# Kernel optimization log

Hardware: AMD Instinct MI355X
Metric: run time of the kernel (lower is better)

The kernel has to match this reference:

```python
import jax, jax.numpy as jnp
import numpy as np

B, K, VDIM, QDIM, NHID, SE_INNER = 8192, 6, 2048, 1024, 1024, 128

def setup_inputs() -> dict:
    key = jax.random.key(0)
    ks = jax.random.split(key, 10)
    w = lambda k, shape: jax.random.normal(k, shape, dtype=jnp.float32) * 0.02
    return {
        "v": jax.random.normal(ks[0], (B, K, VDIM), dtype=jnp.float32),
        "q": jax.random.normal(ks[1], (B, QDIM), dtype=jnp.float32),
        "mask": (jax.random.uniform(ks[2], (B, K)) > 0.5).astype(jnp.float32),
        "W1": w(ks[3], (NHID, VDIM + QDIM)),   # FCNet weight-normed Linear (effective weight)
        "b1": jnp.zeros((NHID,), jnp.float32),
        "Wl": w(ks[4], (1, NHID)),             # logits Linear(num_hid, 1)
        "bl": jnp.zeros((1,), jnp.float32),
        "Wse1": w(ks[5], (SE_INNER, 1)),       # SELayer fc1, no bias
        "Wse2": w(ks[6], (1, SE_INNER)),       # SELayer fc2, no bias
        "Wf": w(ks[7], (VDIM, 1)),             # final_att_proj Linear(1, v_dim)
        "bf": jnp.zeros((VDIM,), jnp.float32),
    }

def reference(v, q, mask, W1, b1, Wl, bl, Wse1, Wse2, Wf, bf):
    Bn, Kn, _ = v.shape
    # logits(v, q): concat q to every object, FCNet (Linear+ReLU), Linear->1 (dropout is identity at eval)
    qe = jnp.broadcast_to(q[:, None, :], (Bn, Kn, q.shape[-1]))
    vq = jnp.concatenate([v, qe], axis=-1)                       # [B,K,vd+qd]
    joint = jax.nn.relu(jnp.einsum('bkf,hf->bkh', vq, W1) + b1)  # [B,K,NHID]
    logits = jnp.einsum('bkh,oh->bko', joint, Wl) + bl           # [B,K,1]
    single_att = jax.nn.softmax(logits, axis=1)
    w = logits                                                   # view(mask_b, 6, -1) is identity here
    w_ctx = w * mask[..., None]                                  # [B,K,1]
    # per-role sum over the 5 complementary roles == total - self (exact complement index sets)
    neigh = jnp.sum(w_ctx, axis=1, keepdims=True) - w_ctx        # [B,K,1]
    x = neigh[..., None]                                         # [B,K,1,1]
    # SE gate: FC(1->128) -> ReLU -> FC(128->1) -> Sigmoid; out = x * (1 - y)
    y = jax.nn.sigmoid(jax.nn.relu(x @ Wse1.T) @ Wse2.T)          # [B,K,1,1]
    gated = x * (1.0 - y)
    # final_att_proj(gated + w[:,role].unsqueeze(-1)) : Linear(1 -> v_dim)
    upd = (gated + w[..., None]) @ Wf.T + bf                     # [B,K,1,VDIM]
    context_erased_att = upd.reshape(Bn * Kn, 1, upd.shape[-1])  # [B*K,1,VDIM]
    return single_att, context_erased_att
```

## Files before the change

kernel.cpp:

```cpp
#include <hip/hip_runtime.h>

#define B_SZ   8192
#define KOBJ   6
#define VD     2048
#define QD     1024
#define NHID_  1024
#define SEIN   128
#define M_TOT  (B_SZ * KOBJ)
#define K_TOT  (VD + QD)

typedef __bf16 bf16x8 __attribute__((ext_vector_type(8)));
typedef float  f32x4  __attribute__((ext_vector_type(4)));
typedef unsigned int uint4v __attribute__((ext_vector_type(4)));

__device__ __forceinline__ unsigned short f2bf(float f) {
    unsigned u = __builtin_bit_cast(unsigned, f);
    u += 0x7fffu + ((u >> 16) & 1u);
    return (unsigned short)(u >> 16);
}

__global__ __launch_bounds__(256) void conv_bf16(const float* __restrict__ src,
                                                 unsigned short* __restrict__ dst,
                                                 int n8) {
    int i = blockIdx.x * 256 + threadIdx.x;
    if (i < n8) {
        float4 f0 = ((const float4*)src)[2 * i];
        float4 f1 = ((const float4*)src)[2 * i + 1];
        uint4v d;
        d[0] = (unsigned)f2bf(f0.x) | ((unsigned)f2bf(f0.y) << 16);
        d[1] = (unsigned)f2bf(f0.z) | ((unsigned)f2bf(f0.w) << 16);
        d[2] = (unsigned)f2bf(f1.x) | ((unsigned)f2bf(f1.y) << 16);
        d[3] = (unsigned)f2bf(f1.z) | ((unsigned)f2bf(f1.w) << 16);
        ((uint4v*)dst)[i] = d;
    }
}

__global__ __launch_bounds__(256) void gemm_q(
    const unsigned short* __restrict__ qb, const unsigned short* __restrict__ W1b,
    const float* __restrict__ b1, float* __restrict__ Gq)
{
    __shared__ unsigned short At[128 * 32];
    __shared__ unsigned short Bt[128 * 32];

    const int tid  = threadIdx.x;
    const int bid  = blockIdx.x;
    const int nb   = bid & 7;
    const int mb   = bid >> 3;
    const int m0   = mb * 128;
    const int n0   = nb * 128;
    const int wave = tid >> 6, lane = tid & 63;
    const int quad = lane >> 4, l16 = lane & 15;
    const int wr   = (wave >> 1) * 64, wc = (wave & 1) * 64;

    const unsigned short* ga[2];
    const unsigned short* gb[2];
    unsigned short* ldsA[2];
    unsigned short* ldsB[2];
    #pragma unroll
    for (int c = 0; c < 2; ++c) {
        int seg = wave * 2 + c;
        int row = seg * 16 + (lane >> 2);
        int ch  = (lane & 3) ^ ((row >> 1) & 3);
        ga[c]   = qb + (size_t)(m0 + row) * QD + ch * 8;
        gb[c]   = W1b + (size_t)(n0 + row) * K_TOT + VD + ch * 8;
        ldsA[c] = &At[seg * 512];
        ldsB[c] = &Bt[seg * 512];
    }

    f32x4 acc[4][4] = {};
    const int swz = (l16 >> 1) & 3;

    for (int kk = 0; kk < QD; kk += 32) {
        __syncthreads();
        #pragma unroll
        for (int c = 0; c < 2; ++c)
            __builtin_amdgcn_global_load_lds(
                (const __attribute__((address_space(1))) void*)(ga[c] + kk),
                (__attribute__((address_space(3))) void*)ldsA[c], 16, 0, 0);
        #pragma unroll
        for (int c = 0; c < 2; ++c)
            __builtin_amdgcn_global_load_lds(
                (const __attribute__((address_space(1))) void*)(gb[c] + kk),
                (__attribute__((address_space(3))) void*)ldsB[c], 16, 0, 0);
        __syncthreads();

        bf16x8 af[4], bfr[4];
        #pragma unroll
        for (int i = 0; i < 4; ++i)
            af[i] = __builtin_bit_cast(bf16x8,
                *(const uint4v*)&At[(wr + i * 16 + l16) * 32 + ((quad ^ swz) * 8)]);
        #pragma unroll
        for (int j = 0; j < 4; ++j)
            bfr[j] = __builtin_bit_cast(bf16x8,
                *(const uint4v*)&Bt[(wc + j * 16 + l16) * 32 + ((quad ^ swz) * 8)]);
        #pragma unroll
        for (int i = 0; i < 4; ++i)
            #pragma unroll
            for (int j = 0; j < 4; ++j)
                acc[i][j] = __builtin_amdgcn_mfma_f32_16x16x32_bf16(af[i], bfr[j], acc[i][j], 0, 0, 0);
    }

    #pragma unroll
    for (int i = 0; i < 4; ++i)
        #pragma unroll
        for (int j = 0; j < 4; ++j) {
            int n = n0 + wc + j * 16 + l16;
            float bv = b1[n];
            #pragma unroll
            for (int r = 0; r < 4; ++r) {
                int m = m0 + wr + i * 16 + quad * 4 + r;
                Gq[(size_t)m * NHID_ + n] = acc[i][j][r] + bv;
            }
        }
}

__global__ __launch_bounds__(256) void gemm_logits(
    const unsigned short* __restrict__ vb, const unsigned short* __restrict__ W1b,
    const float* __restrict__ Gq, const float* __restrict__ Wl,
    float* __restrict__ logits)
{
    __shared__ unsigned short At[128 * 32];
    __shared__ unsigned short Bt[128 * 32];

    const int tid  = threadIdx.x;
    const int bid  = blockIdx.x;
    const int nb   = bid & 7;
    const int mb   = bid >> 3;
    const int m0   = mb * 128;
    const int n0   = nb * 128;
    const int wave = tid >> 6, lane = tid & 63;
    const int quad = lane >> 4, l16 = lane & 15;
    const int wr   = (wave >> 1) * 64, wc = (wave & 1) * 64;

    const unsigned short* gav[2];
    const unsigned short* gb[2];
    unsigned short* ldsA[2];
    unsigned short* ldsB[2];
    #pragma unroll
    for (int c = 0; c < 2; ++c) {
        int seg = wave * 2 + c;
        int row = seg * 16 + (lane >> 2);
        int ch  = (lane & 3) ^ ((row >> 1) & 3);
        gav[c]  = vb + (size_t)(m0 + row) * VD + ch * 8;
        gb[c]   = W1b + (size_t)(n0 + row) * K_TOT + ch * 8;
        ldsA[c] = &At[seg * 512];
        ldsB[c] = &Bt[seg * 512];
    }

    f32x4 acc[4][4] = {};
    const int swz = (l16 >> 1) & 3;

    for (int kk = 0; kk < VD; kk += 32) {
        __syncthreads();
        #pragma unroll
        for (int c = 0; c < 2; ++c)
            __builtin_amdgcn_global_load_lds(
                (const __attribute__((address_space(1))) void*)(gav[c] + kk),
                (__attribute__((address_space(3))) void*)ldsA[c], 16, 0, 0);
        #pragma unroll
        for (int c = 0; c < 2; ++c)
            __builtin_amdgcn_global_load_lds(
                (const __attribute__((address_space(1))) void*)(gb[c] + kk),
                (__attribute__((address_space(3))) void*)ldsB[c], 16, 0, 0);
        __syncthreads();

        bf16x8 af[4], bfr[4];
        #pragma unroll
        for (int i = 0; i < 4; ++i)
            af[i] = __builtin_bit_cast(bf16x8,
                *(const uint4v*)&At[(wr + i * 16 + l16) * 32 + ((quad ^ swz) * 8)]);
        #pragma unroll
        for (int j = 0; j < 4; ++j)
            bfr[j] = __builtin_bit_cast(bf16x8,
                *(const uint4v*)&Bt[(wc + j * 16 + l16) * 32 + ((quad ^ swz) * 8)]);
        #pragma unroll
        for (int i = 0; i < 4; ++i)
            #pragma unroll
            for (int j = 0; j < 4; ++j)
                acc[i][j] = __builtin_amdgcn_mfma_f32_16x16x32_bf16(af[i], bfr[j], acc[i][j], 0, 0, 0);
    }

    #pragma unroll
    for (int i = 0; i < 4; ++i) {
        #pragma unroll
        for (int r = 0; r < 4; ++r) {
            int m = m0 + wr + i * 16 + quad * 4 + r;
            const float* gqr = Gq + (size_t)(m / KOBJ) * NHID_;
            float sum = 0.f;
            #pragma unroll
            for (int j = 0; j < 4; ++j) {
                int n = n0 + wc + j * 16 + l16;
                float h = fmaxf(acc[i][j][r] + gqr[n], 0.f);
                sum = fmaf(h, Wl[n], sum);
            }
            sum += __shfl_xor(sum, 1);
            sum += __shfl_xor(sum, 2);
            sum += __shfl_xor(sum, 4);
            sum += __shfl_xor(sum, 8);
            if (l16 == 0) atomicAdd(&logits[m], sum);
        }
    }
}

__global__ __launch_bounds__(256) void se_kernel(
    const float* __restrict__ logits, const float* __restrict__ mask,
    const float* __restrict__ bl,
    const float* __restrict__ Wse1, const float* __restrict__ Wse2,
    float* __restrict__ out_att, float* __restrict__ s_buf)
{
    int b = blockIdx.x * 256 + threadIdx.x;
    if (b >= B_SZ) return;
    float w[KOBJ];
    float blv = bl[0];
    #pragma unroll
    for (int k = 0; k < KOBJ; ++k) w[k] = logits[b * KOBJ + k] + blv;

    float mx = w[0];
    #pragma unroll
    for (int k = 1; k < KOBJ; ++k) mx = fmaxf(mx, w[k]);
    float e[KOBJ], den = 0.f;
    #pragma unroll
    for (int k = 0; k < KOBJ; ++k) { e[k] = __expf(w[k] - mx); den += e[k]; }
    float rden = 1.f / den;
    #pragma unroll
    for (int k = 0; k < KOBJ; ++k) out_att[b * KOBJ + k] = e[k] * rden;

    float wcm[KOBJ], tot = 0.f;
    #pragma unroll
    for (int k = 0; k < KOBJ; ++k) { wcm[k] = w[k] * mask[b * KOBJ + k]; tot += wcm[k]; }

    #pragma unroll
    for (int k = 0; k < KOBJ; ++k) {
        float x = tot - wcm[k];
        float a = 0.f;
        for (int i = 0; i < SEIN; ++i)
            a = fmaf(fmaxf(x * Wse1[i], 0.f), Wse2[i], a);
        float y = 1.f / (1.f + __expf(-a));
        s_buf[b * KOBJ + k] = x * (1.f - y) + w[k];
    }
}

__global__ __launch_bounds__(256) void out_writer(
    const float* __restrict__ s_buf, const float* __restrict__ Wf,
    const float* __restrict__ bfv, float* __restrict__ out)
{
    int m = blockIdx.x;
    float s = s_buf[m];
    const float4* wf4 = (const float4*)Wf;
    const float4* bf4 = (const float4*)bfv;
    float4* o4 = (float4*)(out + (size_t)m * VD);
    #pragma unroll
    for (int it = 0; it < VD / 4 / 256; ++it) {
        int t = threadIdx.x + it * 256;
        float4 wv = wf4[t], bv = bf4[t];
        float4 r;
        r.x = fmaf(s, wv.x, bv.x);
        r.y = fmaf(s, wv.y, bv.y);
        r.z = fmaf(s, wv.z, bv.z);
        r.w = fmaf(s, wv.w, bv.w);
        o4[t] = r;
    }
}

extern "C" void kernel_launch(void* const* d_in, const int* in_sizes, int n_in,
                              void* d_out, int out_size, void* d_ws, size_t ws_size,
                              hipStream_t stream) {
    const float* v    = (const float*)d_in[0];
    const float* q    = (const float*)d_in[1];
    const float* mask = (const float*)d_in[2];
    const float* W1   = (const float*)d_in[3];
    const float* b1   = (const float*)d_in[4];
    const float* Wl   = (const float*)d_in[5];
    const float* bl   = (const float*)d_in[6];
    const float* Wse1 = (const float*)d_in[7];
    const float* Wse2 = (const float*)d_in[8];
    const float* Wf   = (const float*)d_in[9];
    const float* bfv  = (const float*)d_in[10];
    float* out = (float*)d_out;

    char* ws = (char*)d_ws;
    unsigned short* W1b = (unsigned short*)ws;
    float* logits = (float*)(ws + 6291456);
    float* s_buf  = (float*)(ws + 6291456 + 196608);

    unsigned short* vb = (unsigned short*)((char*)d_out + (size_t)M_TOT * 4);
    unsigned short* qb = (unsigned short*)((char*)d_out + (size_t)M_TOT * 4 + 201326592);
    float* Gq = (float*)((char*)d_out + (size_t)M_TOT * 4 + 201326592 + 16777216);

    hipMemsetAsync(logits, 0, M_TOT * sizeof(float), stream);
    conv_bf16<<<(NHID_ * K_TOT / 8 + 255) / 256, 256, 0, stream>>>(W1, W1b, NHID_ * K_TOT / 8);
    conv_bf16<<<(B_SZ * QD / 8 + 255) / 256, 256, 0, stream>>>(q, qb, B_SZ * QD / 8);
    gemm_q<<<(B_SZ / 128) * (NHID_ / 128), 256, 0, stream>>>(qb, W1b, b1, Gq);
    conv_bf16<<<(M_TOT * VD / 8 + 255) / 256, 256, 0, stream>>>(v, vb, M_TOT * VD / 8);
    gemm_logits<<<(M_TOT / 128) * (NHID_ / 128), 256, 0, stream>>>(vb, W1b, Gq, Wl, logits);
    se_kernel<<<(B_SZ + 255) / 256, 256, 0, stream>>>(logits, mask, bl, Wse1, Wse2, out, s_buf);
    out_writer<<<M_TOT, 256, 0, stream>>>(s_buf, Wf, bfv, out + M_TOT);
}
```

Before: 1.062 ms.

## Fuse fp32-to-bf16 conversion of v into logits GEMM and remap blocks per XCD

Drops the separate pass that converts v to bf16. The logits GEMM now reads fp32 v directly, converts it in registers and writes bf16 into LDS, which removes a 400MB read and 200MB write round trip. Block indices are also remapped so each XCD handles a contiguous range of M tiles and all 8 N tiles, improving L2 reuse of v rows. The trade-off is that A-tile loads become synchronous register loads instead of async global-to-LDS, and each block reads the fp32 v tile for all 8 N blocks, which doubles the bytes per tile compared with the bf16 copy.

Measured after the change: 1.038 ms. -2.2%, faster.

```diff
diff --git a/kernel.cpp b/kernel.cpp
--- a/kernel.cpp
+++ b/kernel.cpp
@@ -11,6 +11,7 @@
 
 typedef __bf16 bf16x8 __attribute__((ext_vector_type(8)));
 typedef float  f32x4  __attribute__((ext_vector_type(4)));
+typedef float  f32x8  __attribute__((ext_vector_type(8)));
 typedef unsigned int uint4v __attribute__((ext_vector_type(4)));
 
 __device__ __forceinline__ unsigned short f2bf(float f) {
@@ -115,7 +116,7 @@
 }
 
 __global__ __launch_bounds__(256) void gemm_logits(
-    const unsigned short* __restrict__ vb, const unsigned short* __restrict__ W1b,
+    const float* __restrict__ v, const unsigned short* __restrict__ W1b,
     const float* __restrict__ Gq, const float* __restrict__ Wl,
     float* __restrict__ logits)
 {
@@ -124,26 +125,28 @@
 
     const int tid  = threadIdx.x;
     const int bid  = blockIdx.x;
-    const int nb   = bid & 7;
-    const int mb   = bid >> 3;
-    const int m0   = mb * 128;
-    const int n0   = nb * 128;
+    const int xcd = bid & 7;
+    const int j   = bid >> 3;
+    const int nb  = j & 7;
+    const int mb  = xcd * 48 + (j >> 3);
+    const int m0  = mb * 128;
+    const int n0  = nb * 128;
     const int wave = tid >> 6, lane = tid & 63;
     const int quad = lane >> 4, l16 = lane & 15;
     const int wr   = (wave >> 1) * 64, wc = (wave & 1) * 64;
 
-    const unsigned short* gav[2];
+    const float* gav[2];
+    unsigned short* ldsAw[2];
     const unsigned short* gb[2];
-    unsigned short* ldsA[2];
     unsigned short* ldsB[2];
     #pragma unroll
     for (int c = 0; c < 2; ++c) {
         int seg = wave * 2 + c;
         int row = seg * 16 + (lane >> 2);
         int ch  = (lane & 3) ^ ((row >> 1) & 3);
-        gav[c]  = vb + (size_t)(m0 + row) * VD + ch * 8;
+        gav[c]  = v + (size_t)(m0 + row) * VD + ch * 8;
+        ldsAw[c] = &At[seg * 512 + lane * 8];
         gb[c]   = W1b + (size_t)(n0 + row) * K_TOT + ch * 8;
-        ldsA[c] = &At[seg * 512];
         ldsB[c] = &Bt[seg * 512];
     }
 
@@ -152,16 +155,26 @@
 
     for (int kk = 0; kk < VD; kk += 32) {
         __syncthreads();
-        #pragma unroll
-        for (int c = 0; c < 2; ++c)
-            __builtin_amdgcn_global_load_lds(
-                (const __attribute__((address_space(1))) void*)(gav[c] + kk),
-                (__attribute__((address_space(3))) void*)ldsA[c], 16, 0, 0);
         #pragma unroll
         for (int c = 0; c < 2; ++c)
             __builtin_amdgcn_global_load_lds(
                 (const __attribute__((address_space(1))) void*)(gb[c] + kk),
                 (__attribute__((address_space(3))) void*)ldsB[c], 16, 0, 0);
+        float4 a0[2], a1[2];
+        #pragma unroll
+        for (int c = 0; c < 2; ++c) {
+            const float4* p = (const float4*)(gav[c] + kk);
+            a0[c] = p[0];
+            a1[c] = p[1];
+        }
+        #pragma unroll
+        for (int c = 0; c < 2; ++c) {
+            f32x8 f;
+            f[0] = a0[c].x; f[1] = a0[c].y; f[2] = a0[c].z; f[3] = a0[c].w;
+            f[4] = a1[c].x; f[5] = a1[c].y; f[6] = a1[c].z; f[7] = a1[c].w;
+            bf16x8 w = __builtin_convertvector(f, bf16x8);
+            *(uint4v*)ldsAw[c] = __builtin_bit_cast(uint4v, w);
+        }
         __syncthreads();
 
         bf16x8 af[4], bfr[4];
@@ -170,14 +183,14 @@
             af[i] = __builtin_bit_cast(bf16x8,
                 *(const uint4v*)&At[(wr + i * 16 + l16) * 32 + ((quad ^ swz) * 8)]);
         #pragma unroll
-        for (int j = 0; j < 4; ++j)
-            bfr[j] = __builtin_bit_cast(bf16x8,
-                *(const uint4v*)&Bt[(wc + j * 16 + l16) * 32 + ((quad ^ swz) * 8)]);
+        for (int j2 = 0; j2 < 4; ++j2)
+            bfr[j2] = __builtin_bit_cast(bf16x8,
+                *(const uint4v*)&Bt[(wc + j2 * 16 + l16) * 32 + ((quad ^ swz) * 8)]);
         #pragma unroll
         for (int i = 0; i < 4; ++i)
             #pragma unroll
-            for (int j = 0; j < 4; ++j)
-                acc[i][j] = __builtin_amdgcn_mfma_f32_16x16x32_bf16(af[i], bfr[j], acc[i][j], 0, 0, 0);
+            for (int j2 = 0; j2 < 4; ++j2)
+                acc[i][j2] = __builtin_amdgcn_mfma_f32_16x16x32_bf16(af[i], bfr[j2], acc[i][j2], 0, 0, 0);
     }
 
     #pragma unroll
@@ -188,9 +201,9 @@
             const float* gqr = Gq + (size_t)(m / KOBJ) * NHID_;
             float sum = 0.f;
             #pragma unroll
-            for (int j = 0; j < 4; ++j) {
-                int n = n0 + wc + j * 16 + l16;
-                float h = fmaxf(acc[i][j][r] + gqr[n], 0.f);
+            for (int j2 = 0; j2 < 4; ++j2) {
+                int n = n0 + wc + j2 * 16 + l16;
+                float h = fmaxf(acc[i][j2][r] + gqr[n], 0.f);
                 sum = fmaf(h, Wl[n], sum);
             }
             sum += __shfl_xor(sum, 1);
@@ -283,7 +296,6 @@
     float* logits = (float*)(ws + 6291456);
     float* s_buf  = (float*)(ws + 6291456 + 196608);
 
-    unsigned short* vb = (unsigned short*)((char*)d_out + (size_t)M_TOT * 4);
     unsigned short* qb = (unsigned short*)((char*)d_out + (size_t)M_TOT * 4 + 201326592);
     float* Gq = (float*)((char*)d_out + (size_t)M_TOT * 4 + 201326592 + 16777216);
 
@@ -291,8 +303,7 @@
     conv_bf16<<<(NHID_ * K_TOT / 8 + 255) / 256, 256, 0, stream>>>(W1, W1b, NHID_ * K_TOT / 8);
     conv_bf16<<<(B_SZ * QD / 8 + 255) / 256, 256, 0, stream>>>(q, qb, B_SZ * QD / 8);
     gemm_q<<<(B_SZ / 128) * (NHID_ / 128), 256, 0, stream>>>(qb, W1b, b1, Gq);
-    conv_bf16<<<(M_TOT * VD / 8 + 255) / 256, 256, 0, stream>>>(v, vb, M_TOT * VD / 8);
-    gemm_logits<<<(M_TOT / 128) * (NHID_ / 128), 256, 0, stream>>>(vb, W1b, Gq, Wl, logits);
+    gemm_logits<<<(M_TOT / 128) * (NHID_ / 128), 256, 0, stream>>>(v, W1b, Gq, Wl, logits);
     se_kernel<<<(B_SZ + 255) / 256, 256, 0, stream>>>(logits, mask, bl, Wse1, Wse2, out, s_buf);
     out_writer<<<M_TOT, 256, 0, stream>>>(s_buf, Wf, bfv, out + M_TOT);
 }
```
